# Kernel optimization log

Hardware: AMD Instinct MI355X
Metric: run time of the kernel (lower is better)

## Reference

```python
import jax, jax.numpy as jnp
import numpy as np
import math

DIM = 1536
NH = 12
HD = 128          # head_dim
C = HD // 2       # 64 complex rope dims
MAX_ATTN = 15 * 880
EPS = 1e-6


def _rope_tables(max_len=1024, d=HD, theta=10000.0):
    # Wan rope_params: freqs = cat([rope(1024, d-4*(d//6)), rope(1024, 2*(d//6)), rope(1024, 2*(d//6))], dim=1)
    d0 = d - 4 * (d // 6)   # 44 -> 22 complex dims (F axis)
    d1 = 2 * (d // 6)       # 42 -> 21 complex dims (H and W axes)
    parts = []
    for dd in (d0, d1, d1):
        inv = 1.0 / theta ** (np.arange(0, dd, 2, dtype=np.float32) / dd)
        parts.append(np.outer(np.arange(max_len, dtype=np.float32), inv))
    ang = np.concatenate(parts, axis=1)                 # [1024, C]
    return np.stack([np.cos(ang), np.sin(ang)], -1)     # [1024, C, 2]


def rmsnorm(x, g, eps=EPS):
    return x * jax.lax.rsqrt(jnp.mean(x * x, axis=-1, keepdims=True) + eps) * g


def rope_apply(xq, f, h, w, freqs, start_frame):
    # xq: [B, S, N, D]; freqs: [1024, C, 2] cos/sin tables; S = f*h*w
    b, s, n, d = xq.shape
    c = d // 2
    s0 = c - 2 * (c // 3)   # F-axis complex dims (22)
    s1 = c // 3             # H/W-axis complex dims (21)
    cos, sin = freqs[..., 0], freqs[..., 1]

    def per_token(tab):
        tf = jnp.broadcast_to(tab[start_frame:start_frame + f, :s0][:, None, None, :], (f, h, w, s0))
        th = jnp.broadcast_to(tab[:h, s0:s0 + s1][None, :, None, :], (f, h, w, s1))
        tw = jnp.broadcast_to(tab[:w, s0 + s1:][None, None, :, :], (f, h, w, s1))
        return jnp.concatenate([tf, th, tw], -1).reshape(1, s, 1, c)

    pc, ps = per_token(cos), per_token(sin)
    xr = xq.reshape(b, s, n, c, 2)
    re, im = xr[..., 0], xr[..., 1]
    out = jnp.stack([re * pc - im * ps, re * ps + im * pc], -1)
    return out.reshape(b, s, n, d)


def _forward(x, wq, bq, wk, bk, wv, bv, wo, bo, gq, gk, freqs, k_cache, v_cache, f, h, w, current_start):
    b, s, _ = x.shape
    frame_seqlen = h * w
    start_frame = current_start // frame_seqlen

    q = rmsnorm(x @ wq.T + bq, gq).reshape(b, s, NH, HD)
    k = rmsnorm(x @ wk.T + bk, gk).reshape(b, s, NH, HD)
    v = (x @ wv.T + bv).reshape(b, s, NH, HD)

    rq = rope_apply(q, f, h, w, freqs, start_frame)
    rk = rope_apply(k, f, h, w, freqs, start_frame)

    current_end = current_start + s
    # cache not full: append new keys/values at [current_start:current_end]
    k_cache = jax.lax.dynamic_update_slice(k_cache, rk, (0, current_start, 0, 0))
    v_cache = jax.lax.dynamic_update_slice(v_cache, v, (0, current_start, 0, 0))

    win_start = max(0, current_end - MAX_ATTN)
    kk = k_cache[:, win_start:current_end]   # [B, Lk, N, D]
    vv = v_cache[:, win_start:current_end]

    scale = 1.0 / math.sqrt(HD)
    scores = jnp.einsum('bqnd,bknd->bnqk', rq, kk) * scale
    attn = jax.nn.softmax(scores, axis=-1)
    out = jnp.einsum('bnqk,bknd->bqnd', attn, vv).reshape(b, s, DIM)
    return out @ wo.T + bo


def setup_inputs() -> dict:
    key = jax.random.key(0)
    ks = jax.random.split(key, 8)
    B, S, CACHE = 1, 880, 18 * 880
    x = jax.random.normal(ks[0], (B, S, DIM), jnp.float32)

    def lin(k):
        k1, k2 = jax.random.split(k)
        wgt = jax.random.normal(k1, (DIM, DIM), jnp.float32) / math.sqrt(DIM)
        bia = jax.random.normal(k2, (DIM,), jnp.float32) * 0.01
        return wgt, bia

    wq, bq = lin(ks[1]); wk, bk = lin(ks[2]); wv, bv = lin(ks[3]); wo, bo = lin(ks[4])
    gq = jnp.ones((DIM,), jnp.float32)
    gk = jnp.ones((DIM,), jnp.float32)
    freqs = jnp.asarray(_rope_tables())
    k_cache = jax.random.normal(ks[5], (B, CACHE, NH, HD), jnp.float32) * 0.5
    v_cache = jax.random.normal(ks[6], (B, CACHE, NH, HD), jnp.float32) * 0.5
    grid_sizes = jnp.array([1, 22, 40], jnp.int32)  # (F, H, W), H*W = 880
    return dict(x=x, wq=wq, bq=bq, wk=wk, bk=bk, wv=wv, bv=bv, wo=wo, bo=bo,
                gq=gq, gk=gk, freqs=freqs, k_cache=k_cache, v_cache=v_cache,
                grid_sizes=grid_sizes, current_start=10560)


def reference(x, wq, bq, wk, bk, wv, bv, wo, bo, gq, gk, freqs, k_cache, v_cache, grid_sizes, current_start):
    f, h, w = (int(grid_sizes[0]), int(grid_sizes[1]), int(grid_sizes[2]))
    return _forward(x, wq, bq, wk, bk, wv, bv, wo, bo, gq, gk, freqs,
                    k_cache, v_cache, f, h, w, int(current_start))
```

## Files before the change

kernel.cpp:

```cpp
#include <hip/hip_runtime.h>

#define NHEADS 12
#define HDIM 128
#define MODEL_DIM 1536
#define MAX_ATTN_W 13200
#define NSPLIT 12

typedef unsigned short u16;
typedef unsigned int u32;
typedef float f32x4 __attribute__((ext_vector_type(4)));
typedef float f32x16 __attribute__((ext_vector_type(16)));
typedef __bf16 bf16x8 __attribute__((ext_vector_type(8)));

static __device__ __forceinline__ u16 f2bf(float f) {
  union { __bf16 h; u16 u; } cv;
  cv.h = (__bf16)f;
  return cv.u;
}
static __device__ __forceinline__ float bf2f(u16 u) {
  union { u32 u; float f; } cv;
  cv.u = ((u32)u) << 16;
  return cv.f;
}

__global__ void k_conv_bf16(const float* __restrict__ src, u16* __restrict__ dst, int n4) {
  int i = blockIdx.x * blockDim.x + threadIdx.x;
  if (i >= n4) return;
  float4 v = ((const float4*)src)[i];
  u32 lo = (u32)f2bf(v.x) | ((u32)f2bf(v.y) << 16);
  u32 hi = (u32)f2bf(v.z) | ((u32)f2bf(v.w) << 16);
  ((uint2*)dst)[i] = make_uint2(lo, hi);
}

__global__ void k_conv_bf16_w4(const float* __restrict__ s0, const float* __restrict__ s1,
                               const float* __restrict__ s2, const float* __restrict__ s3,
                               u16* __restrict__ d0, u16* __restrict__ d1,
                               u16* __restrict__ d2, u16* __restrict__ d3, int n4) {
  int i = blockIdx.x * blockDim.x + threadIdx.x;
  if (i >= n4) return;
  const int which = blockIdx.y;
  const float* src = (which == 0) ? s0 : (which == 1) ? s1 : (which == 2) ? s2 : s3;
  u16* dst = (which == 0) ? d0 : (which == 1) ? d1 : (which == 2) ? d2 : d3;
  float4 v = ((const float4*)src)[i];
  u32 lo = (u32)f2bf(v.x) | ((u32)f2bf(v.y) << 16);
  u32 hi = (u32)f2bf(v.z) | ((u32)f2bf(v.w) << 16);
  ((uint2*)dst)[i] = make_uint2(lo, hi);
}

__global__ void k_build_kold(const float* __restrict__ kc, u16* __restrict__ K_all,
                             const int* __restrict__ csp, int S, int KVcap) {
  const int cs = csp[0];
  const int ce = cs + S;
  int wst = ce - MAX_ATTN_W; if (wst < 0) wst = 0;
  const int oldlen = cs - wst;
  const long per = (long)oldlen * 16;
  const long total = per * NHEADS;
  for (long c = blockIdx.x * (long)blockDim.x + threadIdx.x; c < total;
       c += (long)gridDim.x * blockDim.x) {
    int n = (int)(c / per);
    long r = c - (long)n * per;
    int jo = (int)(r >> 4);
    int dc = ((int)r & 15) * 8;
    const float* s = kc + ((size_t)(wst + jo) * NHEADS + n) * HDIM + dc;
    float4 a = *(const float4*)s;
    float4 b = *(const float4*)(s + 4);
    uint4 o;
    o.x = (u32)f2bf(a.x) | ((u32)f2bf(a.y) << 16);
    o.y = (u32)f2bf(a.z) | ((u32)f2bf(a.w) << 16);
    o.z = (u32)f2bf(b.x) | ((u32)f2bf(b.y) << 16);
    o.w = (u32)f2bf(b.z) | ((u32)f2bf(b.w) << 16);
    *(uint4*)(K_all + ((size_t)n * KVcap + jo) * HDIM + dc) = o;
  }
}

__launch_bounds__(256)
__global__ void k_build_vtold(const float* __restrict__ vc, u16* __restrict__ VT,
                              const int* __restrict__ csp, int S, int KVcap) {
  __shared__ u16 tile[64][130];
  const int cs = csp[0];
  const int ce = cs + S;
  int wst = ce - MAX_ATTN_W; if (wst < 0) wst = 0;
  const int oldlen = cs - wst;
  const int n = blockIdx.y;
  const int j0 = blockIdx.x * 64;
  if (j0 >= oldlen) return;
  const int tid = threadIdx.x;

  #pragma unroll
  for (int i = 0; i < 8; i++) {
    int idx = tid + 256 * i;
    int j = idx >> 5;
    int dc = (idx & 31) * 4;
    float4 v = make_float4(0.f, 0.f, 0.f, 0.f);
    if (j0 + j < oldlen)
      v = *(const float4*)(vc + ((size_t)(wst + j0 + j) * NHEADS + n) * HDIM + dc);
    u32 lo = (u32)f2bf(v.x) | ((u32)f2bf(v.y) << 16);
    u32 hi = (u32)f2bf(v.z) | ((u32)f2bf(v.w) << 16);
    *(u32*)&tile[j][dc] = lo;
    *(u32*)&tile[j][dc + 2] = hi;
  }
  __syncthreads();

  const int d = tid >> 1;
  const int jh = (tid & 1) * 32;
  alignas(16) u16 buf[32];
  #pragma unroll
  for (int j = 0; j < 32; j++) buf[j] = tile[jh + j][d];
  u16* dst = VT + ((size_t)n * HDIM + d) * KVcap + j0 + jh;
  if (j0 + jh + 32 <= oldlen) {
    #pragma unroll
    for (int c = 0; c < 4; c++)
      *(uint4*)(dst + c * 8) = *(const uint4*)&buf[c * 8];
  } else {
    for (int j = 0; j < 32 && j0 + jh + j < oldlen; j++) dst[j] = buf[j];
  }
}

__launch_bounds__(256)
__global__ void k_gemm_bt(const u16* __restrict__ A, const u16* __restrict__ B,
                          const float* __restrict__ bias, float* __restrict__ out,
                          int M, int N, int K) {
  __shared__ __align__(16) u16 Al[64][40];
  __shared__ __align__(16) u16 Bl[64][40];
  const int tid = threadIdx.x;
  const int w = tid >> 6, l = tid & 63, l15 = l & 15, g = l >> 4;
  const int wr = w >> 1, wc = w & 1;
  const int m0 = blockIdx.x * 64, n0 = blockIdx.y * 64;
  f32x4 acc[2][2] = {};
  const int row = tid >> 2, colc = (tid & 3) * 8;
  for (int k0 = 0; k0 < K; k0 += 32) {
    __syncthreads();
    uint4 av = make_uint4(0, 0, 0, 0);
    int gm = m0 + row;
    if (gm < M) av = *(const uint4*)(A + (size_t)gm * K + k0 + colc);
    *(uint4*)&Al[row][colc] = av;
    uint4 bv = *(const uint4*)(B + (size_t)(n0 + row) * K + k0 + colc);
    *(uint4*)&Bl[row][colc] = bv;
    __syncthreads();
    bf16x8 af[2], bfr[2];
    #pragma unroll
    for (int mt = 0; mt < 2; mt++) af[mt] = *(const bf16x8*)&Al[wr * 32 + mt * 16 + l15][g * 8];
    #pragma unroll
    for (int nt = 0; nt < 2; nt++) bfr[nt] = *(const bf16x8*)&Bl[wc * 32 + nt * 16 + l15][g * 8];
    #pragma unroll
    for (int mt = 0; mt < 2; mt++)
      #pragma unroll
      for (int nt = 0; nt < 2; nt++)
        acc[mt][nt] = __builtin_amdgcn_mfma_f32_16x16x32_bf16(af[mt], bfr[nt], acc[mt][nt], 0, 0, 0);
  }
  #pragma unroll
  for (int mt = 0; mt < 2; mt++)
    #pragma unroll
    for (int nt = 0; nt < 2; nt++)
      #pragma unroll
      for (int r = 0; r < 4; r++) {
        int mm = m0 + wr * 32 + mt * 16 + (g << 2) + r;
        int nn = n0 + wc * 32 + nt * 16 + l15;
        if (mm < M) out[(size_t)mm * N + nn] = acc[mt][nt][r] + bias[nn];
      }
}

__launch_bounds__(256)
__global__ void k_gemm_qkv(const u16* __restrict__ A,
                           const u16* __restrict__ B0, const u16* __restrict__ B1,
                           const u16* __restrict__ B2,
                           const float* __restrict__ bias0, const float* __restrict__ bias1,
                           const float* __restrict__ bias2,
                           float* __restrict__ o0, float* __restrict__ o1, float* __restrict__ o2,
                           int M, int N, int K) {
  __shared__ __align__(16) u16 Al[64][40];
  __shared__ __align__(16) u16 Bl[64][40];
  const int nblk = N / 64;
  const int which = blockIdx.y / nblk;
  const int n0 = (blockIdx.y % nblk) * 64;
  const u16* B = (which == 0) ? B0 : ((which == 1) ? B1 : B2);
  const float* bias = (which == 0) ? bias0 : ((which == 1) ? bias1 : bias2);
  float* out = (which == 0) ? o0 : ((which == 1) ? o1 : o2);
  const int tid = threadIdx.x;
  const int w = tid >> 6, l = tid & 63, l15 = l & 15, g = l >> 4;
  const int wr = w >> 1, wc = w & 1;
  const int m0 = blockIdx.x * 64;
  f32x4 acc[2][2] = {};
  const int row = tid >> 2, colc = (tid & 3) * 8;
  for (int k0 = 0; k0 < K; k0 += 32) {
    __syncthreads();
    uint4 av = make_uint4(0, 0, 0, 0);
    int gm = m0 + row;
    if (gm < M) av = *(const uint4*)(A + (size_t)gm * K + k0 + colc);
    *(uint4*)&Al[row][colc] = av;
    uint4 bv = *(const uint4*)(B + (size_t)(n0 + row) * K + k0 + colc);
    *(uint4*)&Bl[row][colc] = bv;
    __syncthreads();
    bf16x8 af[2], bfr[2];
    #pragma unroll
    for (int mt = 0; mt < 2; mt++) af[mt] = *(const bf16x8*)&Al[wr * 32 + mt * 16 + l15][g * 8];
    #pragma unroll
    for (int nt = 0; nt < 2; nt++) bfr[nt] = *(const bf16x8*)&Bl[wc * 32 + nt * 16 + l15][g * 8];
    #pragma unroll
    for (int mt = 0; mt < 2; mt++)
      #pragma unroll
      for (int nt = 0; nt < 2; nt++)
        acc[mt][nt] = __builtin_amdgcn_mfma_f32_16x16x32_bf16(af[mt], bfr[nt], acc[mt][nt], 0, 0, 0);
  }
  #pragma unroll
  for (int mt = 0; mt < 2; mt++)
    #pragma unroll
    for (int nt = 0; nt < 2; nt++)
      #pragma unroll
      for (int r = 0; r < 4; r++) {
        int mm = m0 + wr * 32 + mt * 16 + (g << 2) + r;
        int nn = n0 + wc * 32 + nt * 16 + l15;
        if (mm < M) out[(size_t)mm * N + nn] = acc[mt][nt][r] + bias[nn];
      }
}

__launch_bounds__(256)
__global__ void k_norm_rope(const float* __restrict__ qp, const float* __restrict__ kp,
                            const float* __restrict__ vp, const float* __restrict__ gq,
                            const float* __restrict__ gk, const float* __restrict__ freqs,
                            const int* __restrict__ gs, const int* __restrict__ csp,
                            int S, int KVcap,
                            u16* __restrict__ rq, u16* __restrict__ K_all,
                            u16* __restrict__ VT) {
  const int t = blockIdx.x;
  const int tid = threadIdx.x;
  const float* q = qp + (size_t)t * MODEL_DIM;
  const float* k = kp + (size_t)t * MODEL_DIM;
  const float* v = vp + (size_t)t * MODEL_DIM;
  float sq = 0.f, sk = 0.f;
  for (int j = tid; j < MODEL_DIM; j += 256) {
    float a = q[j]; sq += a * a;
    float b = k[j]; sk += b * b;
  }
  #pragma unroll
  for (int off = 32; off > 0; off >>= 1) {
    sq += __shfl_down(sq, off, 64);
    sk += __shfl_down(sk, off, 64);
  }
  __shared__ float red[8];
  int wv_ = tid >> 6, l = tid & 63;
  if (l == 0) { red[wv_] = sq; red[4 + wv_] = sk; }
  __syncthreads();
  sq = red[0] + red[1] + red[2] + red[3];
  sk = red[4] + red[5] + red[6] + red[7];
  const float rq_s = rsqrtf(sq * (1.0f / MODEL_DIM) + 1e-6f);
  const float rk_s = rsqrtf(sk * (1.0f / MODEL_DIM) + 1e-6f);

  const int cs = csp[0];
  const int h = gs[1], ww = gs[2];
  const int hw = h * ww;
  const int sf = cs / hw;
  const int fi = t / hw;
  const int rr = t - fi * hw;
  const int hi = rr / ww;
  const int wi = rr - hi * ww;
  const int ce = cs + S;
  int wst = ce - MAX_ATTN_W; if (wst < 0) wst = 0;
  const int jj = cs + t - wst;

  for (int p = tid; p < NHEADS * 64; p += 256) {
    int n = p >> 6, c = p & 63;
    int pos = (c < 22) ? (sf + fi) : ((c < 43) ? hi : wi);
    float cv = freqs[(pos * 64 + c) * 2];
    float sv = freqs[(pos * 64 + c) * 2 + 1];
    int j0 = n * HDIM + 2 * c;
    float qr = q[j0] * rq_s * gq[j0];
    float qi = q[j0 + 1] * rq_s * gq[j0 + 1];
    u32 oq = (u32)f2bf(qr * cv - qi * sv) | ((u32)f2bf(qr * sv + qi * cv) << 16);
    *(u32*)(rq + ((size_t)n * S + t) * HDIM + 2 * c) = oq;
    float kr = k[j0] * rk_s * gk[j0];
    float ki = k[j0 + 1] * rk_s * gk[j0 + 1];
    u32 ok = (u32)f2bf(kr * cv - ki * sv) | ((u32)f2bf(kr * sv + ki * cv) << 16);
    *(u32*)(K_all + ((size_t)n * KVcap + jj) * HDIM + 2 * c) = ok;
  }
  for (int j = tid; j < MODEL_DIM; j += 256) {
    int n = j >> 7, d = j & 127;
    VT[((size_t)n * HDIM + d) * KVcap + jj] = f2bf(v[j]);
  }
}

__launch_bounds__(256, 2)
__global__ void k_attn_split(const u16* __restrict__ rq, const u16* __restrict__ K_all,
                             const u16* __restrict__ VT,
                             u16* __restrict__ po, float* __restrict__ pm, float* __restrict__ pl,
                             const int* __restrict__ csp, int S, int KVcap) {
  __shared__ __align__(16) u16 Klds[64][128];
  __shared__ __align__(16) u16 Vlds[128][64];

  const int tid = threadIdx.x;
  const int wid = tid >> 6;
  const int l = tid & 63;
  const int l31 = l & 31;
  const int hi = l >> 5;
  const int swz = (l31 & 7) << 3;
  const int head = blockIdx.y;
  const int split = blockIdx.z;
  const int q0 = blockIdx.x * 128;

  const int cs = csp[0];
  const int ce = cs + S;
  int wst = ce - MAX_ATTN_W; if (wst < 0) wst = 0;
  const int KV = ce - wst;
  const int chunk = (((KV + NSPLIT - 1) / NSPLIT) + 63) & ~63;
  const int kstart = split * chunk;
  int kend = kstart + chunk; if (kend > KV) kend = KV;

  const size_t pbase = ((size_t)head * NSPLIT + split) * S;
  const int qrow = q0 + wid * 32 + l31;

  if (kstart >= kend) {
    if (qrow < S && hi == 0) { pm[pbase + qrow] = -3.0e38f; pl[pbase + qrow] = 0.f; }
    return;
  }

  bf16x8 qf[8];
  if (qrow < S) {
    const u16* qp = rq + ((size_t)head * S + qrow) * HDIM;
    #pragma unroll
    for (int ds = 0; ds < 8; ds++) qf[ds] = *(const bf16x8*)(qp + ds * 16 + hi * 8);
  } else {
    #pragma unroll
    for (int ds = 0; ds < 8; ds++)
      #pragma unroll
      for (int i = 0; i < 8; i++) qf[ds][i] = (__bf16)0.0f;
  }

  f32x16 o[4];
  #pragma unroll
  for (int dt = 0; dt < 4; dt++)
    #pragma unroll
    for (int j = 0; j < 16; j++) o[dt][j] = 0.f;
  float m_ = -3.0e38f, lsum_ = 0.f;

  const u16* Kh = K_all + (size_t)head * KVcap * HDIM;
  const u16* Vh = VT + (size_t)head * HDIM * KVcap;
  const float sc2 = 0.12751744f;

  uint4 kr[4], vr[4];
  auto load_tile = [&](int key0) {
    #pragma unroll
    for (int i = 0; i < 4; i++) {
      int cid = tid + 256 * i;
      int krow = cid >> 4;
      int gk_ = key0 + krow;
      kr[i] = make_uint4(0, 0, 0, 0);
      if (gk_ < kend) kr[i] = *(const uint4*)(Kh + (size_t)gk_ * HDIM + (cid & 15) * 8);
    }
    #pragma unroll
    for (int i = 0; i < 4; i++) {
      int cid = tid + 256 * i;
      int d = cid >> 3;
      int kc = (cid & 7) * 8;
      const u16* src = Vh + (size_t)d * KVcap + key0 + kc;
      if (key0 + kc + 8 <= kend) {
        vr[i] = *(const uint4*)src;
      } else {
        alignas(16) u16 tmp[8];
        #pragma unroll
        for (int j = 0; j < 8; j++) tmp[j] = (key0 + kc + j < kend) ? src[j] : (u16)0;
        vr[i] = *(const uint4*)tmp;
      }
    }
  };

  const int ntiles = (kend - kstart + 63) >> 6;
  load_tile(kstart);

  for (int t = 0; t < ntiles; t++) {
    const int key0 = kstart + (t << 6);
    __syncthreads();
    #pragma unroll
    for (int i = 0; i < 4; i++) {
      int cid = tid + 256 * i;
      int krow = cid >> 4;
      *(uint4*)&Klds[krow][((cid & 15) * 8) ^ ((krow & 7) << 3)] = kr[i];
    }
    #pragma unroll
    for (int i = 0; i < 4; i++) {
      int cid = tid + 256 * i;
      int d = cid >> 3;
      *(uint4*)&Vlds[d][((cid & 7) * 8) ^ ((d & 7) << 3)] = vr[i];
    }
    if (t + 1 < ntiles) load_tile(key0 + 64);
    __syncthreads();

    f32x16 s[2];
    #pragma unroll
    for (int kt = 0; kt < 2; kt++) {
      #pragma unroll
      for (int j = 0; j < 16; j++) s[kt][j] = 0.f;
      #pragma unroll
      for (int ds = 0; ds < 8; ds++) {
        bf16x8 kf = *(const bf16x8*)&Klds[kt * 32 + l31][(ds * 16 + hi * 8) ^ swz];
        s[kt] = __builtin_amdgcn_mfma_f32_32x32x16_bf16(kf, qf[ds], s[kt], 0, 0, 0);
      }
    }

    float tm = -3.0e38f;
    #pragma unroll
    for (int kt = 0; kt < 2; kt++) {
      const int rem = kend - key0 - kt * 32;
      #pragma unroll
      for (int r = 0; r < 16; r++) {
        const int off = (r & 3) + 8 * (r >> 2) + 4 * hi;
        float v = s[kt][r] * sc2;
        v = (off < rem) ? v : -3.0e38f;
        s[kt][r] = v;
        tm = fmaxf(tm, v);
      }
    }
    tm = fmaxf(tm, __shfl_xor(tm, 32, 64));
    float nm = fmaxf(m_, tm);
    float alpha = exp2f(m_ - nm);
    m_ = nm;

    float rs = 0.f;
    u32 w[2][8];
    #pragma unroll
    for (int kt = 0; kt < 2; kt++)
      #pragma unroll
      for (int j = 0; j < 8; j++) {
        float p0 = exp2f(s[kt][2 * j] - m_);
        float p1 = exp2f(s[kt][2 * j + 1] - m_);
        rs += p0 + p1;
        w[kt][j] = (u32)f2bf(p0) | ((u32)f2bf(p1) << 16);
      }
    rs += __shfl_xor(rs, 32, 64);
    lsum_ = lsum_ * alpha + rs;

    union { u32 u[4]; bf16x8 v; } pf[2][2];
    #pragma unroll
    for (int kt = 0; kt < 2; kt++) {
      u32 xw[8];
      #pragma unroll
      for (int j = 0; j < 8; j++) xw[j] = __shfl_xor(w[kt][j], 32, 64);
      pf[kt][0].u[0] = hi ? xw[2]    : w[kt][0];
      pf[kt][0].u[1] = hi ? xw[3]    : w[kt][1];
      pf[kt][0].u[2] = hi ? w[kt][2] : xw[0];
      pf[kt][0].u[3] = hi ? w[kt][3] : xw[1];
      pf[kt][1].u[0] = hi ? xw[6]    : w[kt][4];
      pf[kt][1].u[1] = hi ? xw[7]    : w[kt][5];
      pf[kt][1].u[2] = hi ? w[kt][6] : xw[4];
      pf[kt][1].u[3] = hi ? w[kt][7] : xw[5];
    }

    #pragma unroll
    for (int dt = 0; dt < 4; dt++)
      #pragma unroll
      for (int j = 0; j < 16; j++) o[dt][j] *= alpha;

    #pragma unroll
    for (int dt = 0; dt < 4; dt++) {
      #pragma unroll
      for (int kt = 0; kt < 2; kt++)
        #pragma unroll
        for (int mm = 0; mm < 2; mm++) {
          bf16x8 vf = *(const bf16x8*)&Vlds[dt * 32 + l31][(kt * 32 + mm * 16 + hi * 8) ^ swz];
          o[dt] = __builtin_amdgcn_mfma_f32_32x32x16_bf16(vf, pf[kt][mm].v, o[dt], 0, 0, 0);
        }
    }
  }

  if (qrow < S) {
    float rl = (lsum_ > 0.f) ? (1.0f / lsum_) : 0.f;
    u16* dst = po + (pbase + qrow) * HDIM;
    #pragma unroll
    for (int dt = 0; dt < 4; dt++)
      #pragma unroll
      for (int jj = 0; jj < 4; jj++) {
        u32 w0 = (u32)f2bf(o[dt][4 * jj] * rl) | ((u32)f2bf(o[dt][4 * jj + 1] * rl) << 16);
        u32 w1 = (u32)f2bf(o[dt][4 * jj + 2] * rl) | ((u32)f2bf(o[dt][4 * jj + 3] * rl) << 16);
        *(uint2*)(dst + dt * 32 + 8 * jj + 4 * hi) = make_uint2(w0, w1);
      }
    if (hi == 0) { pm[pbase + qrow] = m_; pl[pbase + qrow] = lsum_; }
  }
}

__global__ void k_attn_reduce(const u16* __restrict__ po, const float* __restrict__ pm,
                              const float* __restrict__ pl, u16* __restrict__ attn_out,
                              int S) {
  const int t = blockIdx.x;
  const int h = blockIdx.y;
  const int d = threadIdx.x;
  float ms[NSPLIT];
  float M = -3.0e38f;
  #pragma unroll
  for (int s = 0; s < NSPLIT; s++) {
    ms[s] = pm[((size_t)h * NSPLIT + s) * S + t];
    M = fmaxf(M, ms[s]);
  }
  float L = 0.f, acc = 0.f;
  #pragma unroll
  for (int s = 0; s < NSPLIT; s++) {
    float wgt = exp2f(ms[s] - M) * pl[((size_t)h * NSPLIT + s) * S + t];
    L += wgt;
    acc += wgt * bf2f(po[(((size_t)h * NSPLIT + s) * S + t) * HDIM + d]);
  }
  attn_out[(size_t)t * MODEL_DIM + h * HDIM + d] = f2bf(acc / L);
}

extern "C" void kernel_launch(void* const* d_in, const int* in_sizes, int n_in,
                              void* d_out, int out_size, void* d_ws, size_t ws_size,
                              hipStream_t stream) {
  (void)n_in; (void)out_size; (void)ws_size;
  const float* x  = (const float*)d_in[0];
  const float* wq = (const float*)d_in[1];
  const float* bq = (const float*)d_in[2];
  const float* wk = (const float*)d_in[3];
  const float* bk = (const float*)d_in[4];
  const float* wv = (const float*)d_in[5];
  const float* bv = (const float*)d_in[6];
  const float* wo = (const float*)d_in[7];
  const float* bo = (const float*)d_in[8];
  const float* gq = (const float*)d_in[9];
  const float* gk = (const float*)d_in[10];
  const float* freqs = (const float*)d_in[11];
  const float* k_cache = (const float*)d_in[12];
  const float* v_cache = (const float*)d_in[13];
  const int* gs  = (const int*)d_in[14];
  const int* csp = (const int*)d_in[15];

  const int S = in_sizes[0] / MODEL_DIM;
  const int CACHE = in_sizes[12] / (NHEADS * HDIM);
  const int KVcap = (CACHE < MAX_ATTN_W) ? CACHE : MAX_ATTN_W;

  char* ws = (char*)d_ws;
  size_t off = 0;
  auto alloc = [&](size_t bytes) {
    char* p = ws + off;
    off += (bytes + 255) & ~(size_t)255;
    return p;
  };
  u16* xb   = (u16*)alloc((size_t)S * MODEL_DIM * 2);
  u16* wqb  = (u16*)alloc((size_t)MODEL_DIM * MODEL_DIM * 2);
  u16* wkb  = (u16*)alloc((size_t)MODEL_DIM * MODEL_DIM * 2);
  u16* wvb  = (u16*)alloc((size_t)MODEL_DIM * MODEL_DIM * 2);
  u16* wob  = (u16*)alloc((size_t)MODEL_DIM * MODEL_DIM * 2);
  float* q_pre = (float*)alloc((size_t)S * MODEL_DIM * 4);
  float* k_pre = (float*)alloc((size_t)S * MODEL_DIM * 4);
  float* v_pre = (float*)alloc((size_t)S * MODEL_DIM * 4);
  u16* rqb   = (u16*)alloc((size_t)NHEADS * S * HDIM * 2);
  u16* K_all = (u16*)alloc((size_t)NHEADS * KVcap * HDIM * 2);
  u16* VT    = (u16*)alloc((size_t)NHEADS * HDIM * KVcap * 2);
  u16* attn_o = (u16*)alloc((size_t)S * MODEL_DIM * 2);
  u16* po    = (u16*)alloc((size_t)NHEADS * NSPLIT * S * HDIM * 2);
  float* pm  = (float*)alloc((size_t)NHEADS * NSPLIT * S * 4);
  float* pl  = (float*)alloc((size_t)NHEADS * NSPLIT * S * 4);

  const int nx4 = S * MODEL_DIM / 4;
  const int nw4 = MODEL_DIM * MODEL_DIM / 4;
  hipLaunchKernelGGL(k_conv_bf16, dim3((nx4 + 255) / 256), dim3(256), 0, stream, x, xb, nx4);
  hipLaunchKernelGGL(k_conv_bf16_w4, dim3((nw4 + 255) / 256, 4), dim3(256), 0, stream,
                     wq, wk, wv, wo, wqb, wkb, wvb, wob, nw4);

  hipLaunchKernelGGL(k_build_kold, dim3(2048), dim3(256), 0, stream, k_cache, K_all, csp, S, KVcap);
  hipLaunchKernelGGL(k_build_vtold, dim3((KVcap + 63) / 64, NHEADS), dim3(256), 0, stream,
                     v_cache, VT, csp, S, KVcap);

  hipLaunchKernelGGL(k_gemm_qkv, dim3((S + 63) / 64, 3 * MODEL_DIM / 64), dim3(256), 0, stream,
                     xb, wqb, wkb, wvb, bq, bk, bv, q_pre, k_pre, v_pre, S, MODEL_DIM, MODEL_DIM);

  hipLaunchKernelGGL(k_norm_rope, dim3(S), dim3(256), 0, stream,
                     q_pre, k_pre, v_pre, gq, gk, freqs, gs, csp, S, KVcap, rqb, K_all, VT);

  hipLaunchKernelGGL(k_attn_split, dim3((S + 127) / 128, NHEADS, NSPLIT), dim3(256), 0, stream,
                     rqb, K_all, VT, po, pm, pl, csp, S, KVcap);

  hipLaunchKernelGGL(k_attn_reduce, dim3(S, NHEADS), dim3(128), 0, stream, po, pm, pl, attn_o, S);

  hipLaunchKernelGGL(k_gemm_bt, dim3((S + 63) / 64, MODEL_DIM / 64), dim3(256), 0, stream,
                     attn_o, wob, bo, (float*)d_out, S, MODEL_DIM, MODEL_DIM);
}
```

Before: 326.5 us.

## Enlarge QKV GEMM tiles, fold softmax scale into Q, lazy rescale in attention

The QKV GEMM moves from 64x64 tiles with 16x16 MFMA to 128x128 tiles with 32x32x16 MFMA, and the activation buffer is padded to a multiple of 128 rows so A loads need no bounds check. The softmax scale is folded into the Q normalisation, which removes a per-score multiply in attention. Masking now runs only on the last partial key tile, and the online-softmax rescale is skipped unless the max grows by more than 8 (in log2 units), which saves ALU work in the inner loop. Attention launch bounds rise to 3 blocks per CU, which may spill registers. The padded rows of xb are read without being written, but those output rows are guarded and discarded.

```diff
diff --git a/kernel.cpp b/kernel.cpp
--- a/kernel.cpp
+++ b/kernel.cpp
@@ -161,57 +161,72 @@
 }
 
 __launch_bounds__(256)
-__global__ void k_gemm_qkv(const u16* __restrict__ A,
-                           const u16* __restrict__ B0, const u16* __restrict__ B1,
-                           const u16* __restrict__ B2,
-                           const float* __restrict__ bias0, const float* __restrict__ bias1,
-                           const float* __restrict__ bias2,
-                           float* __restrict__ o0, float* __restrict__ o1, float* __restrict__ o2,
-                           int M, int N, int K) {
-  __shared__ __align__(16) u16 Al[64][40];
-  __shared__ __align__(16) u16 Bl[64][40];
-  const int nblk = N / 64;
+__global__ void k_gemm_qkv128(const u16* __restrict__ A,
+                              const u16* __restrict__ B0, const u16* __restrict__ B1,
+                              const u16* __restrict__ B2,
+                              const float* __restrict__ bias0, const float* __restrict__ bias1,
+                              const float* __restrict__ bias2,
+                              float* __restrict__ o0, float* __restrict__ o1, float* __restrict__ o2,
+                              int M, int N, int K) {
+  __shared__ __align__(16) u16 Al[128][40];
+  __shared__ __align__(16) u16 Bl[128][40];
+  const int nblk = N / 128;
   const int which = blockIdx.y / nblk;
-  const int n0 = (blockIdx.y % nblk) * 64;
+  const int n0 = (blockIdx.y % nblk) * 128;
   const u16* B = (which == 0) ? B0 : ((which == 1) ? B1 : B2);
   const float* bias = (which == 0) ? bias0 : ((which == 1) ? bias1 : bias2);
   float* out = (which == 0) ? o0 : ((which == 1) ? o1 : o2);
   const int tid = threadIdx.x;
-  const int w = tid >> 6, l = tid & 63, l15 = l & 15, g = l >> 4;
-  const int wr = w >> 1, wc = w & 1;
-  const int m0 = blockIdx.x * 64;
-  f32x4 acc[2][2] = {};
+  const int wid = tid >> 6, l = tid & 63, l31 = l & 31, hi = l >> 5;
+  const int wr = wid >> 1, wc = wid & 1;
+  const int m0 = blockIdx.x * 128;
+  f32x16 acc[2][2];
+  #pragma unroll
+  for (int mt = 0; mt < 2; mt++)
+    #pragma unroll
+    for (int nt = 0; nt < 2; nt++)
+      #pragma unroll
+      for (int j = 0; j < 16; j++) acc[mt][nt][j] = 0.f;
   const int row = tid >> 2, colc = (tid & 3) * 8;
   for (int k0 = 0; k0 < K; k0 += 32) {
     __syncthreads();
-    uint4 av = make_uint4(0, 0, 0, 0);
-    int gm = m0 + row;
-    if (gm < M) av = *(const uint4*)(A + (size_t)gm * K + k0 + colc);
-    *(uint4*)&Al[row][colc] = av;
-    uint4 bv = *(const uint4*)(B + (size_t)(n0 + row) * K + k0 + colc);
-    *(uint4*)&Bl[row][colc] = bv;
+    uint4 a0 = *(const uint4*)(A + (size_t)(m0 + row) * K + k0 + colc);
+    uint4 a1 = *(const uint4*)(A + (size_t)(m0 + row + 64) * K + k0 + colc);
+    uint4 b0 = *(const uint4*)(B + (size_t)(n0 + row) * K + k0 + colc);
+    uint4 b1 = *(const uint4*)(B + (size_t)(n0 + row + 64) * K + k0 + colc);
+    *(uint4*)&Al[row][colc] = a0;
+    *(uint4*)&Al[row + 64][colc] = a1;
+    *(uint4*)&Bl[row][colc] = b0;
+    *(uint4*)&Bl[row + 64][colc] = b1;
     __syncthreads();
-    bf16x8 af[2], bfr[2];
-    #pragma unroll
-    for (int mt = 0; mt < 2; mt++) af[mt] = *(const bf16x8*)&Al[wr * 32 + mt * 16 + l15][g * 8];
-    #pragma unroll
-    for (int nt = 0; nt < 2; nt++) bfr[nt] = *(const bf16x8*)&Bl[wc * 32 + nt * 16 + l15][g * 8];
-    #pragma unroll
-    for (int mt = 0; mt < 2; mt++)
+    #pragma unroll
+    for (int ks = 0; ks < 2; ks++) {
+      bf16x8 af[2], bfr[2];
+      #pragma unroll
+      for (int mt = 0; mt < 2; mt++)
+        af[mt] = *(const bf16x8*)&Al[wr * 64 + mt * 32 + l31][ks * 16 + hi * 8];
       #pragma unroll
       for (int nt = 0; nt < 2; nt++)
-        acc[mt][nt] = __builtin_amdgcn_mfma_f32_16x16x32_bf16(af[mt], bfr[nt], acc[mt][nt], 0, 0, 0);
+        bfr[nt] = *(const bf16x8*)&Bl[wc * 64 + nt * 32 + l31][ks * 16 + hi * 8];
+      #pragma unroll
+      for (int mt = 0; mt < 2; mt++)
+        #pragma unroll
+        for (int nt = 0; nt < 2; nt++)
+          acc[mt][nt] = __builtin_amdgcn_mfma_f32_32x32x16_bf16(af[mt], bfr[nt], acc[mt][nt], 0, 0, 0);
+    }
   }
   #pragma unroll
   for (int mt = 0; mt < 2; mt++)
     #pragma unroll
-    for (int nt = 0; nt < 2; nt++)
-      #pragma unroll
-      for (int r = 0; r < 4; r++) {
-        int mm = m0 + wr * 32 + mt * 16 + (g << 2) + r;
-        int nn = n0 + wc * 32 + nt * 16 + l15;
-        if (mm < M) out[(size_t)mm * N + nn] = acc[mt][nt][r] + bias[nn];
-      }
+    for (int nt = 0; nt < 2; nt++) {
+      const int col = n0 + wc * 64 + nt * 32 + l31;
+      const float bb = bias[col];
+      #pragma unroll
+      for (int r = 0; r < 16; r++) {
+        int rowo = m0 + wr * 64 + mt * 32 + (r & 3) + 8 * (r >> 2) + 4 * hi;
+        if (rowo < M) out[(size_t)rowo * N + col] = acc[mt][nt][r] + bb;
+      }
+    }
 }
 
 __launch_bounds__(256)
@@ -243,7 +258,7 @@
   __syncthreads();
   sq = red[0] + red[1] + red[2] + red[3];
   sk = red[4] + red[5] + red[6] + red[7];
-  const float rq_s = rsqrtf(sq * (1.0f / MODEL_DIM) + 1e-6f);
+  const float rq_s = rsqrtf(sq * (1.0f / MODEL_DIM) + 1e-6f) * 0.12751744f;
   const float rk_s = rsqrtf(sk * (1.0f / MODEL_DIM) + 1e-6f);
 
   const int cs = csp[0];
@@ -279,7 +294,7 @@
   }
 }
 
-__launch_bounds__(256, 2)
+__launch_bounds__(256, 3)
 __global__ void k_attn_split(const u16* __restrict__ rq, const u16* __restrict__ K_all,
                              const u16* __restrict__ VT,
                              u16* __restrict__ po, float* __restrict__ pm, float* __restrict__ pl,
@@ -334,7 +349,6 @@
 
   const u16* Kh = K_all + (size_t)head * KVcap * HDIM;
   const u16* Vh = VT + (size_t)head * HDIM * KVcap;
-  const float sc2 = 0.12751744f;
 
   uint4 kr[4], vr[4];
   auto load_tile = [&](int key0) {
@@ -397,22 +411,36 @@
     }
 
     float tm = -3.0e38f;
-    #pragma unroll
-    for (int kt = 0; kt < 2; kt++) {
-      const int rem = kend - key0 - kt * 32;
-      #pragma unroll
-      for (int r = 0; r < 16; r++) {
-        const int off = (r & 3) + 8 * (r >> 2) + 4 * hi;
-        float v = s[kt][r] * sc2;
-        v = (off < rem) ? v : -3.0e38f;
-        s[kt][r] = v;
-        tm = fmaxf(tm, v);
+    if (key0 + 64 <= kend) {
+      #pragma unroll
+      for (int kt = 0; kt < 2; kt++)
+        #pragma unroll
+        for (int r = 0; r < 16; r++) tm = fmaxf(tm, s[kt][r]);
+    } else {
+      #pragma unroll
+      for (int kt = 0; kt < 2; kt++) {
+        const int rem = kend - key0 - kt * 32;
+        #pragma unroll
+        for (int r = 0; r < 16; r++) {
+          const int off = (r & 3) + 8 * (r >> 2) + 4 * hi;
+          float v = (off < rem) ? s[kt][r] : -3.0e38f;
+          s[kt][r] = v;
+          tm = fmaxf(tm, v);
+        }
       }
     }
     tm = fmaxf(tm, __shfl_xor(tm, 32, 64));
-    float nm = fmaxf(m_, tm);
-    float alpha = exp2f(m_ - nm);
-    m_ = nm;
+
+    if (!__all(tm <= m_ + 8.0f)) {
+      float nm = fmaxf(m_, tm);
+      float alpha = exp2f(m_ - nm);
+      m_ = nm;
+      lsum_ *= alpha;
+      #pragma unroll
+      for (int dt = 0; dt < 4; dt++)
+        #pragma unroll
+        for (int j = 0; j < 16; j++) o[dt][j] *= alpha;
+    }
 
     float rs = 0.f;
     u32 w[2][8];
@@ -426,7 +454,7 @@
         w[kt][j] = (u32)f2bf(p0) | ((u32)f2bf(p1) << 16);
       }
     rs += __shfl_xor(rs, 32, 64);
-    lsum_ = lsum_ * alpha + rs;
+    lsum_ += rs;
 
     union { u32 u[4]; bf16x8 v; } pf[2][2];
     #pragma unroll
@@ -443,11 +471,6 @@
       pf[kt][1].u[2] = hi ? w[kt][6] : xw[4];
       pf[kt][1].u[3] = hi ? w[kt][7] : xw[5];
     }
-
-    #pragma unroll
-    for (int dt = 0; dt < 4; dt++)
-      #pragma unroll
-      for (int j = 0; j < 16; j++) o[dt][j] *= alpha;
 
     #pragma unroll
     for (int dt = 0; dt < 4; dt++) {
@@ -523,6 +546,7 @@
   const int S = in_sizes[0] / MODEL_DIM;
   const int CACHE = in_sizes[12] / (NHEADS * HDIM);
   const int KVcap = (CACHE < MAX_ATTN_W) ? CACHE : MAX_ATTN_W;
+  const int Mpad = (S + 127) & ~127;
 
   char* ws = (char*)d_ws;
   size_t off = 0;
@@ -531,7 +555,7 @@
     off += (bytes + 255) & ~(size_t)255;
     return p;
   };
-  u16* xb   = (u16*)alloc((size_t)S * MODEL_DIM * 2);
+  u16* xb   = (u16*)alloc((size_t)Mpad * MODEL_DIM * 2);
   u16* wqb  = (u16*)alloc((size_t)MODEL_DIM * MODEL_DIM * 2);
   u16* wkb  = (u16*)alloc((size_t)MODEL_DIM * MODEL_DIM * 2);
   u16* wvb  = (u16*)alloc((size_t)MODEL_DIM * MODEL_DIM * 2);
@@ -557,7 +581,7 @@
   hipLaunchKernelGGL(k_build_vtold, dim3((KVcap + 63) / 64, NHEADS), dim3(256), 0, stream,
                      v_cache, VT, csp, S, KVcap);
 
-  hipLaunchKernelGGL(k_gemm_qkv, dim3((S + 63) / 64, 3 * MODEL_DIM / 64), dim3(256), 0, stream,
+  hipLaunchKernelGGL(k_gemm_qkv128, dim3(Mpad / 128, 3 * MODEL_DIM / 128), dim3(256), 0, stream,
                      xb, wqb, wkb, wvb, bq, bk, bv, q_pre, k_pre, v_pre, S, MODEL_DIM, MODEL_DIM);
 
   hipLaunchKernelGGL(k_norm_rope, dim3(S), dim3(256), 0, stream,
```

After: 703.4 us. 2.15x slower.
